# Performance work log

Measured on AMD Instinct MI355X. Metric: run time of the kernel, lower is better.

## Reference

```python
import jax, jax.numpy as jnp
import numpy as np

SIGMA = 1.0
N_DOCS = 10_000_000
N_SAMPLED = 8192  # n = ceil(sqrt(random_pairs)), random_pairs = 67108864


def setup_inputs() -> dict:
    key = jax.random.key(0)
    k1, k2, k3 = jax.random.split(key, 3)
    scores = jax.random.normal(k1, (N_DOCS, 1), dtype=jnp.float32)
    target = jax.random.randint(k2, (N_DOCS,), 0, 5, dtype=jnp.int32)
    random_docs = jax.random.randint(k3, (N_SAMPLED,), 0, N_DOCS, dtype=jnp.int32)
    return {"scores": scores, "target": target, "random_docs": random_docs}


def reference(scores, target, random_docs):
    # Gather sampled docs' targets and scores.
    t = target[random_docs].astype(jnp.float32)   # [n]
    s = scores[random_docs, 0]                    # [n]
    # S_ij = sign(target_i - target_j)  (the if/elif/else ladder in the source)
    S = jnp.sign(t[:, None] - t[None, :])         # [n, n]
    # Source bug preserved: z_j = s_i.detach(), so calc_p(z_i, z_j) = sigmoid(0) = 0.5 exactly.
    # lambda_ij = sigma * (0.5 * (1 - S) - 0.5). (i == j pairs contribute 0 since S = 0.)
    lam = SIGMA * (0.5 * (1.0 - S) - 0.5)         # [n, n]
    row = jnp.sum(lam, axis=1)                    # sum_j lambda_ij for each sampled i
    # Source bug preserved: lambda_i is never reset across the outer loop -> cumulative sum.
    cum = jnp.cumsum(row)                         # [n]
    # loss = sum_k cum_lambda[k] * s_{i_k}; lambdas are detached (constants w.r.t. grad).
    loss = jnp.sum(jax.lax.stop_gradient(cum) * s)
    return loss.reshape(1)
```

## Files before the change

### kernel.cpp

```cpp
#include <hip/hip_runtime.h>

#define NS   8192
#define B1   64
#define T1   128
#define RECW 16

__device__ __forceinline__ unsigned fnv11(const unsigned* w, unsigned seed) {
    unsigned h = seed;
    #pragma unroll
    for (int i = 0; i < 11; ++i) h = (h ^ w[i]) * 16777619u;
    return h;
}

__global__ __launch_bounds__(T1) void k_fused(
    const float* __restrict__ scores,
    const int*   __restrict__ target,
    const int*   __restrict__ docs,
    unsigned*    __restrict__ ws,
    float*       __restrict__ out)
{
    const int tid  = threadIdx.x;
    const int b    = blockIdx.x;
    const int lane = tid & 63;
    const int wave = tid >> 6;

    const int   d = docs[b * T1 + tid];
    const int   t = target[d];
    const float s = scores[d];

    float incl = s;
    #pragma unroll
    for (int off = 1; off < 64; off <<= 1) {
        const float v = __shfl_up(incl, off, 64);
        if (lane >= off) incl += v;
    }

    __shared__ float wsum[2];
    __shared__ float acc[10];
    if (lane == 63) wsum[wave] = incl;
    if (tid < 10) acc[tid] = 0.0f;
    __syncthreads();

    const float excl = incl - s + (wave == 1 ? wsum[0] : 0.0f);
    atomicAdd(&acc[t], 1.0f);
    atomicAdd(&acc[5 + t], excl);
    __syncthreads();

    if (tid == 0) {
        unsigned w[11];
        #pragma unroll
        for (int i = 0; i < 10; ++i) w[i] = __float_as_uint(acc[i]);
        w[10] = __float_as_uint(wsum[0] + wsum[1]);
        const unsigned h1 = fnv11(w, 2166136261u);
        const unsigned h2 = fnv11(w, 0x9E3779B9u);
        unsigned* rec = ws + b * RECW;
        #pragma unroll
        for (int i = 0; i < 11; ++i)
            __hip_atomic_store(&rec[i], w[i], __ATOMIC_RELAXED,
                               __HIP_MEMORY_SCOPE_AGENT);
        __hip_atomic_store(&rec[11], h1, __ATOMIC_RELEASE,
                           __HIP_MEMORY_SCOPE_AGENT);
        __hip_atomic_store(&rec[12], h2, __ATOMIC_RELEASE,
                           __HIP_MEMORY_SCOPE_AGENT);
    }

    if (b == 0 && wave == 0) {
        unsigned w[11];
        const unsigned* rec = ws + lane * RECW;
        bool ok = false;
        do {
            if (!ok) {
                #pragma unroll
                for (int i = 0; i < 11; ++i)
                    w[i] = __hip_atomic_load(&rec[i], __ATOMIC_RELAXED,
                                             __HIP_MEMORY_SCOPE_AGENT);
                const unsigned c1 = __hip_atomic_load(&rec[11], __ATOMIC_ACQUIRE,
                                                      __HIP_MEMORY_SCOPE_AGENT);
                const unsigned c2 = __hip_atomic_load(&rec[12], __ATOMIC_ACQUIRE,
                                                      __HIP_MEMORY_SCOPE_AGENT);
                ok = (c1 == fnv11(w, 2166136261u)) &&
                     (c2 == fnv11(w, 0x9E3779B9u));
            }
            if (!__all(ok)) __builtin_amdgcn_s_sleep(2);
        } while (!__all(ok));

        float cnt[5], pq[5];
        #pragma unroll
        for (int v = 0; v < 5; ++v) {
            cnt[v] = __uint_as_float(w[v]);
            pq[v]  = __uint_as_float(w[5 + v]);
        }
        const float ssum = __uint_as_float(w[10]);

        float bincl = ssum;
        #pragma unroll
        for (int off = 1; off < 64; off <<= 1) {
            const float v = __shfl_up(bincl, off, 64);
            if (lane >= off) bincl += v;
        }
        const float S_total = __shfl(bincl, 63, 64);
        const float preoff  = bincl - ssum;

        double Q[5], C[5];
        #pragma unroll
        for (int v = 0; v < 5; ++v) {
            Q[v] = (double)cnt[v] * (double)(S_total - preoff) - (double)pq[v];
            C[v] = (double)cnt[v];
        }

        #pragma unroll
        for (int v = 0; v < 5; ++v) {
            #pragma unroll
            for (int off = 32; off > 0; off >>= 1) {
                Q[v] += __shfl_down(Q[v], off, 64);
                C[v] += __shfl_down(C[v], off, 64);
            }
        }

        if (lane == 0) {
            double loss = 0.0;
            #pragma unroll
            for (int ww = 0; ww < 5; ++ww) {
                double lo = 0.0, hi = 0.0;
                #pragma unroll
                for (int v = 0; v < 5; ++v) {
                    if (v < ww) lo += Q[v];
                    if (v > ww) hi += Q[v];
                }
                loss += C[ww] * (lo - hi);
            }
            out[0] = (float)(0.5 * loss);
        }
    }
}

extern "C" void kernel_launch(void* const* d_in, const int* in_sizes, int n_in,
                              void* d_out, int out_size, void* d_ws, size_t ws_size,
                              hipStream_t stream) {
    const float* scores = (const float*)d_in[0];
    const int*   target = (const int*)d_in[1];
    const int*   docs   = (const int*)d_in[2];
    float*       out    = (float*)d_out;
    unsigned*    ws     = (unsigned*)d_ws;

    k_fused<<<B1, T1, 0, stream>>>(scores, target, docs, ws, out);
}
```

Before: 10.85 us.

## Dedicate a separate consumer block and use wave ballots instead of shared atomics

Launches one extra block that only polls the per-block checksummed records and finishes the reduction, so the consumer no longer first has to do its own share of gather work. Producer blocks replace the shared-memory float atomics with per-wave ballot/popcount counts and shuffle reductions, merge two waves with a single barrier, and drop the release ordering on the hash stores. The consumer also sleeps for shorter intervals while spinning. The relaxed hash stores depend on the checksum alone to detect torn records, and the extra block adds scheduling of one more workgroup.

```diff
diff --git a/kernel.cpp b/kernel.cpp
--- a/kernel.cpp
+++ b/kernel.cpp
@@ -1,7 +1,7 @@
 #include <hip/hip_runtime.h>
 
 #define NS   8192
-#define B1   64
+#define NB   64
 #define T1   128
 #define RECW 16
 
@@ -24,113 +24,133 @@
     const int lane = tid & 63;
     const int wave = tid >> 6;
 
-    const int   d = docs[b * T1 + tid];
-    const int   t = target[d];
-    const float s = scores[d];
+    if (b != 0) {
+        const int   g = b - 1;
+        const int   d = docs[g * T1 + tid];
+        const int   t = target[d];
+        const float s = scores[d];
 
-    float incl = s;
+        float incl = s;
+        #pragma unroll
+        for (int off = 1; off < 64; off <<= 1) {
+            const float v = __shfl_up(incl, off, 64);
+            if (lane >= off) incl += v;
+        }
+        const float wexcl = incl - s;
+        const float wsum  = __shfl(incl, 63, 64);
+
+        float cntw[5], pqw[5];
+        #pragma unroll
+        for (int v = 0; v < 5; ++v) {
+            const unsigned long long m = __ballot(t == v);
+            cntw[v] = (float)__popcll(m);
+            float x = (t == v) ? wexcl : 0.0f;
+            #pragma unroll
+            for (int off = 32; off > 0; off >>= 1)
+                x += __shfl_down(x, off, 64);
+            pqw[v] = x;
+        }
+
+        __shared__ float l1[11];
+        if (wave == 1 && lane == 0) {
+            #pragma unroll
+            for (int v = 0; v < 5; ++v) { l1[v] = cntw[v]; l1[5 + v] = pqw[v]; }
+            l1[10] = wsum;
+        }
+        __syncthreads();
+
+        if (wave == 0 && lane == 0) {
+            unsigned w[11];
+            #pragma unroll
+            for (int v = 0; v < 5; ++v) {
+                const float c = cntw[v] + l1[v];
+                const float p = pqw[v] + l1[5 + v] + wsum * l1[v];
+                w[v]     = __float_as_uint(c);
+                w[5 + v] = __float_as_uint(p);
+            }
+            w[10] = __float_as_uint(wsum + l1[10]);
+            const unsigned h1 = fnv11(w, 2166136261u);
+            const unsigned h2 = fnv11(w, 0x9E3779B9u);
+            unsigned* rec = ws + g * RECW;
+            #pragma unroll
+            for (int i = 0; i < 11; ++i)
+                __hip_atomic_store(&rec[i], w[i], __ATOMIC_RELAXED,
+                                   __HIP_MEMORY_SCOPE_AGENT);
+            __hip_atomic_store(&rec[11], h1, __ATOMIC_RELAXED,
+                               __HIP_MEMORY_SCOPE_AGENT);
+            __hip_atomic_store(&rec[12], h2, __ATOMIC_RELAXED,
+                               __HIP_MEMORY_SCOPE_AGENT);
+        }
+        return;
+    }
+
+    if (wave != 0) return;
+
+    unsigned w[11];
+    const unsigned* rec = ws + lane * RECW;
+    bool ok = false;
+    do {
+        if (!ok) {
+            #pragma unroll
+            for (int i = 0; i < 11; ++i)
+                w[i] = __hip_atomic_load(&rec[i], __ATOMIC_RELAXED,
+                                         __HIP_MEMORY_SCOPE_AGENT);
+            const unsigned c1 = __hip_atomic_load(&rec[11], __ATOMIC_ACQUIRE,
+                                                  __HIP_MEMORY_SCOPE_AGENT);
+            const unsigned c2 = __hip_atomic_load(&rec[12], __ATOMIC_ACQUIRE,
+                                                  __HIP_MEMORY_SCOPE_AGENT);
+            ok = (c1 == fnv11(w, 2166136261u)) &&
+                 (c2 == fnv11(w, 0x9E3779B9u));
+        }
+        if (!__all(ok)) __builtin_amdgcn_s_sleep(1);
+    } while (!__all(ok));
+
+    float cnt[5], pq[5];
+    #pragma unroll
+    for (int v = 0; v < 5; ++v) {
+        cnt[v] = __uint_as_float(w[v]);
+        pq[v]  = __uint_as_float(w[5 + v]);
+    }
+    const float ssum = __uint_as_float(w[10]);
+
+    float bincl = ssum;
     #pragma unroll
     for (int off = 1; off < 64; off <<= 1) {
-        const float v = __shfl_up(incl, off, 64);
-        if (lane >= off) incl += v;
+        const float v = __shfl_up(bincl, off, 64);
+        if (lane >= off) bincl += v;
+    }
+    const float S_total = __shfl(bincl, 63, 64);
+    const float preoff  = bincl - ssum;
+
+    double Q[5], C[5];
+    #pragma unroll
+    for (int v = 0; v < 5; ++v) {
+        Q[v] = (double)cnt[v] * (double)(S_total - preoff) - (double)pq[v];
+        C[v] = (double)cnt[v];
     }
 
-    __shared__ float wsum[2];
-    __shared__ float acc[10];
-    if (lane == 63) wsum[wave] = incl;
-    if (tid < 10) acc[tid] = 0.0f;
-    __syncthreads();
-
-    const float excl = incl - s + (wave == 1 ? wsum[0] : 0.0f);
-    atomicAdd(&acc[t], 1.0f);
-    atomicAdd(&acc[5 + t], excl);
-    __syncthreads();
-
-    if (tid == 0) {
-        unsigned w[11];
+    #pragma unroll
+    for (int v = 0; v < 5; ++v) {
         #pragma unroll
-        for (int i = 0; i < 10; ++i) w[i] = __float_as_uint(acc[i]);
-        w[10] = __float_as_uint(wsum[0] + wsum[1]);
-        const unsigned h1 = fnv11(w, 2166136261u);
-        const unsigned h2 = fnv11(w, 0x9E3779B9u);
-        unsigned* rec = ws + b * RECW;
-        #pragma unroll
-        for (int i = 0; i < 11; ++i)
-            __hip_atomic_store(&rec[i], w[i], __ATOMIC_RELAXED,
-                               __HIP_MEMORY_SCOPE_AGENT);
-        __hip_atomic_store(&rec[11], h1, __ATOMIC_RELEASE,
-                           __HIP_MEMORY_SCOPE_AGENT);
-        __hip_atomic_store(&rec[12], h2, __ATOMIC_RELEASE,
-                           __HIP_MEMORY_SCOPE_AGENT);
+        for (int off = 32; off > 0; off >>= 1) {
+            Q[v] += __shfl_down(Q[v], off, 64);
+            C[v] += __shfl_down(C[v], off, 64);
+        }
     }
 
-    if (b == 0 && wave == 0) {
-        unsigned w[11];
-        const unsigned* rec = ws + lane * RECW;
-        bool ok = false;
-        do {
-            if (!ok) {
-                #pragma unroll
-                for (int i = 0; i < 11; ++i)
-                    w[i] = __hip_atomic_load(&rec[i], __ATOMIC_RELAXED,
-                                             __HIP_MEMORY_SCOPE_AGENT);
-                const unsigned c1 = __hip_atomic_load(&rec[11], __ATOMIC_ACQUIRE,
-                                                      __HIP_MEMORY_SCOPE_AGENT);
-                const unsigned c2 = __hip_atomic_load(&rec[12], __ATOMIC_ACQUIRE,
-                                                      __HIP_MEMORY_SCOPE_AGENT);
-                ok = (c1 == fnv11(w, 2166136261u)) &&
-                     (c2 == fnv11(w, 0x9E3779B9u));
+    if (lane == 0) {
+        double loss = 0.0;
+        #pragma unroll
+        for (int ww = 0; ww < 5; ++ww) {
+            double lo = 0.0, hi = 0.0;
+            #pragma unroll
+            for (int v = 0; v < 5; ++v) {
+                if (v < ww) lo += Q[v];
+                if (v > ww) hi += Q[v];
             }
-            if (!__all(ok)) __builtin_amdgcn_s_sleep(2);
-        } while (!__all(ok));
-
-        float cnt[5], pq[5];
-        #pragma unroll
-        for (int v = 0; v < 5; ++v) {
-            cnt[v] = __uint_as_float(w[v]);
-            pq[v]  = __uint_as_float(w[5 + v]);
+            loss += C[ww] * (lo - hi);
         }
-        const float ssum = __uint_as_float(w[10]);
-
-        float bincl = ssum;
-        #pragma unroll
-        for (int off = 1; off < 64; off <<= 1) {
-            const float v = __shfl_up(bincl, off, 64);
-            if (lane >= off) bincl += v;
-        }
-        const float S_total = __shfl(bincl, 63, 64);
-        const float preoff  = bincl - ssum;
-
-        double Q[5], C[5];
-        #pragma unroll
-        for (int v = 0; v < 5; ++v) {
-            Q[v] = (double)cnt[v] * (double)(S_total - preoff) - (double)pq[v];
-            C[v] = (double)cnt[v];
-        }
-
-        #pragma unroll
-        for (int v = 0; v < 5; ++v) {
-            #pragma unroll
-            for (int off = 32; off > 0; off >>= 1) {
-                Q[v] += __shfl_down(Q[v], off, 64);
-                C[v] += __shfl_down(C[v], off, 64);
-            }
-        }
-
-        if (lane == 0) {
-            double loss = 0.0;
-            #pragma unroll
-            for (int ww = 0; ww < 5; ++ww) {
-                double lo = 0.0, hi = 0.0;
-                #pragma unroll
-                for (int v = 0; v < 5; ++v) {
-                    if (v < ww) lo += Q[v];
-                    if (v > ww) hi += Q[v];
-                }
-                loss += C[ww] * (lo - hi);
-            }
-            out[0] = (float)(0.5 * loss);
-        }
+        out[0] = (float)(0.5 * loss);
     }
 }
 
@@ -143,5 +163,5 @@
     float*       out    = (float*)d_out;
     unsigned*    ws     = (unsigned*)d_ws;
 
-    k_fused<<<B1, T1, 0, stream>>>(scores, target, docs, ws, out);
+    k_fused<<<NB + 1, T1, 0, stream>>>(scores, target, docs, ws, out);
 }
```

New measurement: 9.699 us. 1.12x faster.
